# Kernel optimization log

Measured on AMD Instinct MI355X. Metric: run time of the kernel, lower is better.

The kernel has to match this reference:

```python
import jax, jax.numpy as jnp
import numpy as np

DIM = 1024
HEADS = 8
DIM_HEAD = 128
SCALE = DIM_HEAD ** -0.5
EPS = 1e-10
ROPE_THETA = 10000.0


def _rope_cos_sin(n, d, dtype):
    # lucidrains rotary-embedding-torch: interleaved freqs, repeated pairwise
    inv_freq = 1.0 / (ROPE_THETA ** (jnp.arange(0, d, 2, dtype=jnp.float32) / d))
    freqs = jnp.arange(n, dtype=jnp.float32)[:, None] * inv_freq[None, :]  # [n, d/2]
    freqs = jnp.repeat(freqs, 2, axis=-1)  # [n, d] interleaved (f0,f0,f1,f1,...)
    return jnp.cos(freqs).astype(dtype), jnp.sin(freqs).astype(dtype)


def _rotate_half(x):
    x = x.reshape(*x.shape[:-1], -1, 2)
    x1, x2 = x[..., 0], x[..., 1]
    return jnp.stack((-x2, x1), axis=-1).reshape(*x.shape[:-2], -1)


def _apply_rope(t, cos, sin):
    return t * cos + _rotate_half(t) * sin


def setup_inputs() -> dict:
    key = jax.random.key(0)
    k1, k2, k3, k4, k5 = jax.random.split(key, 5)
    b, n = 2, 2048
    return {
        "x": jax.random.normal(k1, (b, n, DIM), dtype=jnp.float32),
        "gamma": jnp.ones((DIM,), dtype=jnp.float32),
        "w_qkv": jax.random.normal(k2, (3 * HEADS * DIM_HEAD, DIM), dtype=jnp.float32) * 0.02,
        "w_out": jax.random.normal(k3, (DIM, HEADS * DIM_HEAD), dtype=jnp.float32) * 0.02,
        "head_gates": jnp.ones((HEADS,), dtype=jnp.float32) * 10.0,
        "mem_kv": jax.random.normal(k4, (b, HEADS, DIM_HEAD, DIM_HEAD), dtype=jnp.float32),
        "mem_norm": jax.random.uniform(k5, (b, HEADS, DIM_HEAD), dtype=jnp.float32) + 0.5,
    }


def _retrieve(t, mem_kv, mem_norm):
    # t: [b,h,n,dk] -> [b,h,n,dv]
    numer = jnp.einsum('bhnk,bhkv->bhnv', t, mem_kv)
    denom = jnp.einsum('bhnk,bhk->bhn', t, mem_norm)
    return numer / jnp.clip(denom, EPS, None)[..., None]


def reference(x, gamma, w_qkv, w_out, head_gates, mem_kv, mem_norm):
    b, n, _ = x.shape
    # RMSNorm (F.normalize * sqrt(dim) * gamma)
    xn = x / jnp.clip(jnp.linalg.norm(x, axis=-1, keepdims=True), 1e-12, None)
    xn = xn * (DIM ** 0.5) * gamma
    # qkv projection, split heads: 'b n (qkv h d) -> qkv b h n d'
    qkv = xn @ w_qkv.T  # [b,n,3*h*d]
    qkv = qkv.reshape(b, n, 3, HEADS, DIM_HEAD).transpose(2, 0, 3, 1, 4)
    q, k, v = qkv[0], qkv[1], qkv[2]

    cos, sin = _rope_cos_sin(n, DIM_HEAD, x.dtype)
    q_rot = _apply_rope(q * SCALE, cos, sin)
    k_rot = _apply_rope(k, cos, sin)

    sim = jnp.einsum('bhid,bhjd->bhij', q_rot, k_rot)
    causal = jnp.triu(jnp.ones((n, n), dtype=bool), 1)
    sim = jnp.where(causal, jnp.finfo(sim.dtype).min, sim)
    attn = jax.nn.softmax(sim, axis=-1)
    out = jnp.einsum('bhij,bhjd->bhid', attn, v)

    # linear-attention feature map on UNrotated, unscaled q/k
    qf = jax.nn.elu(q) + 1.0
    kf = jax.nn.elu(k) + 1.0

    # gated retrieval from past memories
    mem_out = _retrieve(qf, mem_kv, mem_norm)
    gates = jax.nn.sigmoid(head_gates)[None, :, None, None]
    out = out * gates + mem_out * (1.0 - gates)

    out = out.transpose(0, 2, 1, 3).reshape(b, n, HEADS * DIM_HEAD)
    out = out @ w_out.T

    # delta rule memory update
    delta_v = _retrieve(kf, mem_kv, mem_norm)
    v_new = v - delta_v
    new_kv = jnp.einsum('bhnk,bhnv->bhkv', kf, v_new) + mem_kv
    new_norm = kf.sum(axis=2) + mem_norm
    return out, new_kv, new_norm
```

## Files before the change

kernel.cpp:

```cpp
#include <hip/hip_runtime.h>
#include <hip/hip_bf16.h>

#define B_ 2
#define N_ 2048
#define H_ 8
#define DH_ 128
#define D_ 1024
#define NO_ 3072
#define SCALE_ 0.08838834764831845f

typedef __bf16 bf16;
typedef __bf16 bf16x4 __attribute__((ext_vector_type(4)));
typedef __bf16 bf16x8 __attribute__((ext_vector_type(8)));
typedef float f32x4 __attribute__((ext_vector_type(4)));

__device__ inline f32x4 mfma16(bf16x8 a, bf16x8 b, f32x4 c) {
  return __builtin_amdgcn_mfma_f32_16x16x32_bf16(a, b, c, 0, 0, 0);
}

__device__ inline float elu1(float x) { return x > 0.f ? x + 1.f : __expf(x); }

__device__ inline void gl_lds16(const bf16* g, bf16* l) {
  __builtin_amdgcn_global_load_lds(
      (const __attribute__((address_space(1))) unsigned int*)g,
      (__attribute__((address_space(3))) unsigned int*)l, 16, 0, 0);
}

__global__ __launch_bounds__(256) void k_rmsnorm(const float* __restrict__ x,
                                                 const float* __restrict__ gamma,
                                                 bf16* __restrict__ xn) {
  int row = blockIdx.x;
  int t = threadIdx.x;
  const float4* xr = (const float4*)(x + (size_t)row * D_);
  float4 xv = xr[t];
  float ss = xv.x*xv.x + xv.y*xv.y + xv.z*xv.z + xv.w*xv.w;
#pragma unroll
  for (int m = 1; m < 64; m <<= 1) ss += __shfl_xor(ss, m);
  __shared__ float sred[4];
  if ((t & 63) == 0) sred[t >> 6] = ss;
  __syncthreads();
  float tot = sred[0] + sred[1] + sred[2] + sred[3];
  float scale = 32.0f / fmaxf(sqrtf(tot), 1e-12f);
  float4 gv = ((const float4*)gamma)[t];
  bf16x4 ov;
  ov[0] = (bf16)(xv.x * scale * gv.x);
  ov[1] = (bf16)(xv.y * scale * gv.y);
  ov[2] = (bf16)(xv.z * scale * gv.z);
  ov[3] = (bf16)(xv.w * scale * gv.w);
  *(bf16x4*)(xn + (size_t)row * D_ + t * 4) = ov;
}

__global__ void k_cvt4(const float4* __restrict__ in, bf16x4* __restrict__ out, int n4) {
  int i = blockIdx.x * blockDim.x + threadIdx.x;
  if (i < n4) {
    float4 v = in[i];
    bf16x4 o;
    o[0] = (bf16)v.x; o[1] = (bf16)v.y; o[2] = (bf16)v.z; o[3] = (bf16)v.w;
    out[i] = o;
  }
}

__global__ __launch_bounds__(256) void k_mkvT(const float* __restrict__ mem_kv,
                                              bf16* __restrict__ mkvT) {
  int bh = blockIdx.x;
  int t = threadIdx.x;
  int v = t & 127, khalf = t >> 7;
  const float* src = mem_kv + (size_t)bh * DH_ * DH_;
  bf16* dst = mkvT + (size_t)bh * DH_ * DH_ + (size_t)v * DH_ + khalf * 64;
#pragma unroll
  for (int kk8 = 0; kk8 < 8; kk8++) {
    int k0 = khalf * 64 + kk8 * 8;
    bf16x8 o;
#pragma unroll
    for (int e = 0; e < 8; e++) o[e] = (bf16)src[(size_t)(k0 + e) * DH_ + v];
    *(bf16x8*)(dst + kk8 * 8) = o;
  }
}

template <typename OT>
__global__ __launch_bounds__(256) void k_gemm_lds(const bf16* __restrict__ A,
                                                  const bf16* __restrict__ B,
                                                  OT* __restrict__ C,
                                                  int M, int Nn, int K) {
  __shared__ __align__(16) bf16 sA[128 * 32];
  __shared__ __align__(16) bf16 sB[128 * 32];
  int t = threadIdx.x;
  int w = t >> 6, lane = t & 63, quad = lane >> 4, l16 = lane & 15;
  int m0 = blockIdx.y * 128, n0 = blockIdx.x * 128;
  int wr = (w & 1) * 64, wc = (w >> 1) * 64;
  f32x4 zf = {0.f, 0.f, 0.f, 0.f};
  f32x4 acc[4][4];
#pragma unroll
  for (int a = 0; a < 4; a++)
#pragma unroll
    for (int c = 0; c < 4; c++) acc[a][c] = zf;
  int srow = w * 16 + (lane >> 2);
  int scol = (lane & 3) * 8;
  const bf16* gA = A + (size_t)(m0 + srow) * K + scol;
  const bf16* gB = B + (size_t)(n0 + srow) * K + scol;
  bf16* lA0 = sA + (size_t)w * 16 * 32;
  bf16* lA1 = sA + (size_t)(64 + w * 16) * 32;
  bf16* lB0 = sB + (size_t)w * 16 * 32;
  bf16* lB1 = sB + (size_t)(64 + w * 16) * 32;
  for (int k0 = 0; k0 < K; k0 += 32) {
    __syncthreads();
    gl_lds16(gA + k0, lA0);
    gl_lds16(gA + (size_t)64 * K + k0, lA1);
    gl_lds16(gB + k0, lB0);
    gl_lds16(gB + (size_t)64 * K + k0, lB1);
    __syncthreads();
    bf16x8 af[4], bfr[4];
#pragma unroll
    for (int mt = 0; mt < 4; mt++)
      af[mt] = *(const bf16x8*)(sA + (wr + mt * 16 + l16) * 32 + quad * 8);
#pragma unroll
    for (int nt = 0; nt < 4; nt++)
      bfr[nt] = *(const bf16x8*)(sB + (wc + nt * 16 + l16) * 32 + quad * 8);
#pragma unroll
    for (int mt = 0; mt < 4; mt++)
#pragma unroll
      for (int nt = 0; nt < 4; nt++)
        acc[mt][nt] = mfma16(af[mt], bfr[nt], acc[mt][nt]);
  }
#pragma unroll
  for (int mt = 0; mt < 4; mt++)
#pragma unroll
    for (int nt = 0; nt < 4; nt++) {
      int row = m0 + wr + mt * 16 + quad * 4;
      int col = n0 + wc + nt * 16 + l16;
      OT* cp = C + (size_t)row * Nn + col;
#pragma unroll
      for (int r = 0; r < 4; r++) cp[(size_t)r * Nn] = (OT)acc[mt][nt][r];
    }
}

__global__ __launch_bounds__(256) void k_prep2(const bf16* __restrict__ qkv,
                                               const float* __restrict__ mem_norm,
                                               bf16* __restrict__ qr, bf16* __restrict__ kr,
                                               bf16* __restrict__ vT, bf16* __restrict__ kfT,
                                               float* __restrict__ qden, float* __restrict__ kden) {
  __shared__ __align__(16) bf16 sQ[64 * 136], sK[64 * 136], sV[64 * 136];
  __shared__ float smn[128];
  int n0 = blockIdx.x * 64, h = blockIdx.y, b = blockIdx.z;
  size_t bh = (size_t)b * H_ + h;
  int t = threadIdx.x;
#pragma unroll
  for (int p = 0; p < 4; p++) {
    int i = p * 256 + t;
    int row = i >> 4, c16 = i & 15;
    size_t base = ((size_t)b * N_ + n0 + row) * NO_ + (size_t)h * DH_;
    ((uint4*)sQ)[row * 17 + c16] = *((const uint4*)(qkv + base) + c16);
    ((uint4*)sK)[row * 17 + c16] = *((const uint4*)(qkv + base + D_) + c16);
    ((uint4*)sV)[row * 17 + c16] = *((const uint4*)(qkv + base + 2 * D_) + c16);
  }
  if (t < 128) smn[t] = mem_norm[bh * DH_ + t];
  __syncthreads();
  int row = t >> 1, h2 = t & 1, d0 = h2 * 64;
  int n = n0 + row;
  float sq = 0.f, sk = 0.f;
  const float cexp = 13.287712379549449f / 128.0f;
#pragma unroll 2
  for (int c = 0; c < 8; c++) {
    bf16x8 q8 = *(const bf16x8*)(sQ + row * 136 + d0 + c * 8);
    bf16x8 k8 = *(const bf16x8*)(sK + row * 136 + d0 + c * 8);
    bf16x8 qo, ko, kf8;
#pragma unroll
    for (int e = 0; e < 8; e += 2) {
      int d = d0 + c * 8 + e;
      float invf = exp2f(-(float)d * cexp);
      float ang = (float)n * invf;
      float sn, cs;
      __sincosf(ang, &sn, &cs);
      float qx = (float)q8[e] * SCALE_, qy = (float)q8[e + 1] * SCALE_;
      qo[e]     = (bf16)(qx * cs - qy * sn);
      qo[e + 1] = (bf16)(qy * cs + qx * sn);
      float kx = (float)k8[e], ky = (float)k8[e + 1];
      ko[e]     = (bf16)(kx * cs - ky * sn);
      ko[e + 1] = (bf16)(ky * cs + kx * sn);
      float f0 = elu1(kx), f1 = elu1(ky);
      kf8[e] = (bf16)f0; kf8[e + 1] = (bf16)f1;
      sk += f0 * smn[d] + f1 * smn[d + 1];
      sq += elu1((float)q8[e]) * smn[d] + elu1((float)q8[e + 1]) * smn[d + 1];
    }
    *(bf16x8*)(qr + (bh * N_ + n) * DH_ + d0 + c * 8) = qo;
    *(bf16x8*)(kr + (bh * N_ + n) * DH_ + d0 + c * 8) = ko;
    *(bf16x8*)(sK + row * 136 + d0 + c * 8) = kf8;
  }
  sq += __shfl_xor(sq, 1);
  sk += __shfl_xor(sk, 1);
  if (h2 == 0) { qden[bh * N_ + n] = sq; kden[bh * N_ + n] = sk; }
  __syncthreads();
  int d = t >> 1, part = t & 1;
#pragma unroll
  for (int v8 = 0; v8 < 4; v8++) {
    bf16x8 okf, ov;
#pragma unroll
    for (int e = 0; e < 8; e++) {
      int nn = part * 32 + v8 * 8 + e;
      okf[e] = sK[nn * 136 + d];
      ov[e]  = sV[nn * 136 + d];
    }
    size_t o = (bh * DH_ + d) * N_ + n0 + part * 32 + v8 * 8;
    *(bf16x8*)(kfT + o) = okf;
    *(bf16x8*)(vT + o)  = ov;
  }
}

__global__ __launch_bounds__(256) void k_attn2(const bf16* __restrict__ qr,
                                               const bf16* __restrict__ kr,
                                               const bf16* __restrict__ vT,
                                               bf16* __restrict__ attn_out,
                                               bf16* __restrict__ pO,
                                               float* __restrict__ pstat) {
  __shared__ __align__(16) bf16 sK[64 * 128];
  __shared__ __align__(16) bf16 sV[128 * 64];
  int L = blockIdx.x;
  int x = (L & 7) * 160 + (L >> 3);
  size_t bh = x / 80;
  int e = x % 80;
  int qt, c;
  if (e < 32)      { qt = 31 - (e >> 2); c = e & 3; }
  else if (e < 56) { int u = e - 32; qt = 23 - u / 3; c = u % 3; }
  else if (e < 72) { int u = e - 56; qt = 15 - (u >> 1); c = u & 1; }
  else             { qt = 7 - (e - 72); c = 0; }
  int jt0 = c * 8;
  int jt1 = min(jt0 + 8, qt + 1);

  int t = threadIdx.x;
  int w = t >> 6, lane = t & 63, quad = lane >> 4, l16 = lane & 15;
  int qlo = qt * 64 + w * 16;

  bf16x8 qfrag[4];
  const bf16* qrow = qr + (bh * N_ + qlo + l16) * DH_;
#pragma unroll
  for (int s = 0; s < 4; s++) qfrag[s] = *(const bf16x8*)(qrow + s * 32 + quad * 8);

  f32x4 zf = {0.f, 0.f, 0.f, 0.f};
  f32x4 o[8];
#pragma unroll
  for (int i = 0; i < 8; i++) o[i] = zf;
  float mrow = -1e30f, lrow = 0.f;

  int krow = lane >> 4, kc16 = lane & 15;
  int vrow = lane >> 3, vc8 = lane & 7;

  for (int jt = jt0; jt < jt1; jt++) {
    __syncthreads();
#pragma unroll
    for (int j = 0; j < 4; j++) {
      int prow = w * 16 + j * 4 + krow;
      int grow = (prow & 32) | ((prow & 12) << 1) | ((prow & 16) >> 2) | (prow & 3);
      const bf16* src = kr + (bh * N_ + (size_t)jt * 64 + grow) * DH_ + (kc16 ^ (prow & 7)) * 8;
      gl_lds16(src, sK + (w * 16 + j * 4) * 128);
    }
#pragma unroll
    for (int j = 0; j < 4; j++) {
      int row = w * 32 + j * 8 + vrow;
      const bf16* src = vT + (bh * DH_ + row) * N_ + (size_t)jt * 64 + (vc8 ^ (row & 7)) * 8;
      gl_lds16(src, sV + (w * 32 + j * 8) * 64);
    }
    __syncthreads();

    f32x4 sf[4];
#pragma unroll
    for (int nt = 0; nt < 4; nt++) sf[nt] = zf;
    __builtin_amdgcn_s_setprio(1);
#pragma unroll
    for (int s = 0; s < 4; s++) {
#pragma unroll
      for (int nt = 0; nt < 4; nt++) {
        int row = nt * 16 + l16;
        bf16x8 kf = *(const bf16x8*)(sK + row * 128 + ((s * 32 + quad * 8) ^ ((row & 7) << 3)));
        sf[nt] = mfma16(kf, qfrag[s], sf[nt]);
      }
    }
    __builtin_amdgcn_s_setprio(0);
    if (jt == qt) {
      int qg = qlo + l16;
#pragma unroll
      for (int nt = 0; nt < 4; nt++) {
        int kb = jt * 64 + ((nt >> 1) << 5) + (quad << 3) + ((nt & 1) << 2);
#pragma unroll
        for (int r = 0; r < 4; r++) {
          if (kb + r > qg) sf[nt][r] = -1e30f;
        }
      }
    }
    float tm = -1e30f;
#pragma unroll
    for (int nt = 0; nt < 4; nt++)
#pragma unroll
      for (int r = 0; r < 4; r++) tm = fmaxf(tm, sf[nt][r]);
    tm = fmaxf(tm, __shfl_xor(tm, 16));
    tm = fmaxf(tm, __shfl_xor(tm, 32));
    float mn = fmaxf(mrow, tm);
    float alpha = __expf(mrow - mn);
    float rs = 0.f;
#pragma unroll
    for (int nt = 0; nt < 4; nt++)
#pragma unroll
      for (int r = 0; r < 4; r++) {
        float p = __expf(sf[nt][r] - mn);
        sf[nt][r] = p;
        rs += p;
      }
    rs += __shfl_xor(rs, 16);
    rs += __shfl_xor(rs, 32);
    lrow = lrow * alpha + rs;
    mrow = mn;
#pragma unroll
    for (int i = 0; i < 8; i++) {
      o[i][0] *= alpha; o[i][1] *= alpha;
      o[i][2] *= alpha; o[i][3] *= alpha;
    }
    bf16x8 pa0, pa1;
#pragma unroll
    for (int r = 0; r < 4; r++) {
      pa0[r]     = (bf16)sf[0][r];
      pa0[4 + r] = (bf16)sf[1][r];
      pa1[r]     = (bf16)sf[2][r];
      pa1[4 + r] = (bf16)sf[3][r];
    }
    __builtin_amdgcn_s_setprio(1);
#pragma unroll
    for (int vt = 0; vt < 8; vt++) {
      int row0 = vt * 16 + l16;
      bf16x8 b0 = *(const bf16x8*)(sV + row0 * 64 + ((quad * 8) ^ ((row0 & 7) << 3)));
      bf16x8 b1 = *(const bf16x8*)(sV + row0 * 64 + ((32 + quad * 8) ^ ((row0 & 7) << 3)));
      o[vt] = mfma16(b0, pa0, o[vt]);
      o[vt] = mfma16(b1, pa1, o[vt]);
    }
    __builtin_amdgcn_s_setprio(0);
  }

  if (qt < 8) {
    float inv = 1.f / lrow;
    int qg = qlo + l16;
#pragma unroll
    for (int vt = 0; vt < 8; vt++) {
      bf16x4 ov;
#pragma unroll
      for (int r = 0; r < 4; r++) ov[r] = (bf16)(o[vt][r] * inv);
      *(bf16x4*)(attn_out + (bh * N_ + qg) * DH_ + vt * 16 + quad * 4) = ov;
    }
  } else {
    int cid = ((int)bh * 24 + qt - 8) * 4 + c;
    int lr = w * 16 + l16;
    if (quad == 0) {
      float2 st = {mrow, lrow};
      *(float2*)(pstat + ((size_t)cid * 64 + lr) * 2) = st;
    }
#pragma unroll
    for (int vt = 0; vt < 8; vt++) {
      bf16x4 ov;
#pragma unroll
      for (int r = 0; r < 4; r++) ov[r] = (bf16)o[vt][r];
      *(bf16x4*)(pO + ((size_t)cid * 64 + lr) * DH_ + vt * 16 + quad * 4) = ov;
    }
  }
}

__global__ __launch_bounds__(256) void k_combine(const bf16* __restrict__ pO,
                                                 const float* __restrict__ pstat,
                                                 bf16* __restrict__ attn_out) {
  int x = blockIdx.x;
  int bh = x / 24, qi = x % 24;
  int qt = 8 + qi;
  int nch = (qt + 8) / 8;
  int t = threadIdx.x;
  int row = t >> 2, dseg = (t & 3) * 32;
  int cidb = (bh * 24 + qi) * 4;
  float ms[4], ls[4];
  float mg = -1e30f;
#pragma unroll 4
  for (int c = 0; c < nch; c++) {
    float2 st = *(const float2*)(pstat + ((size_t)(cidb + c) * 64 + row) * 2);
    ms[c] = st.x; ls[c] = st.y;
    mg = fmaxf(mg, st.x);
  }
  float L = 0.f, wc[4];
#pragma unroll 4
  for (int c = 0; c < nch; c++) { wc[c] = __expf(ms[c] - mg); L += ls[c] * wc[c]; }
  float inv = 1.f / L;
  float acc[32];
#pragma unroll
  for (int i = 0; i < 32; i++) acc[i] = 0.f;
#pragma unroll 4
  for (int c = 0; c < nch; c++) {
    const bf16x8* p = (const bf16x8*)(pO + ((size_t)(cidb + c) * 64 + row) * DH_ + dseg);
#pragma unroll
    for (int j = 0; j < 4; j++) {
      bf16x8 v = p[j];
#pragma unroll
      for (int e2 = 0; e2 < 8; e2++) acc[j * 8 + e2] += wc[c] * (float)v[e2];
    }
  }
  bf16* dst = attn_out + ((size_t)bh * N_ + qt * 64 + row) * DH_ + dseg;
#pragma unroll
  for (int j = 0; j < 4; j++) {
    bf16x8 ov;
#pragma unroll
    for (int e2 = 0; e2 < 8; e2++) ov[e2] = (bf16)(acc[j * 8 + e2] * inv);
    *(bf16x8*)(dst + j * 8) = ov;
  }
}

#define SMT_STRIDE 136
#define VNSTR 138
__global__ __launch_bounds__(256) void k_retrieve2(const bf16* __restrict__ qkv,
                                                   const bf16* __restrict__ mkvT,
                                                   const float* __restrict__ qden,
                                                   const float* __restrict__ kden,
                                                   const bf16* __restrict__ attn,
                                                   const float* __restrict__ hg,
                                                   bf16* __restrict__ comb,
                                                   bf16* __restrict__ vnT) {
  __shared__ __align__(16) bf16 smT[DH_ * SMT_STRIDE];
  __shared__ bf16 sVn[64 * VNSTR];
  int h = blockIdx.y, b = blockIdx.z;
  size_t bh = (size_t)b * H_ + h;
  int t = threadIdx.x;
  int w = t >> 6, lane = t & 63, quad = lane >> 4, l16 = lane & 15;
  int n0 = blockIdx.x * 64;

  {
    const uint4* src = (const uint4*)(mkvT + bh * DH_ * DH_);
    uint4* dst = (uint4*)smT;
#pragma unroll
    for (int it = 0; it < 8; it++) {
      int i = t + it * 256;
      int row = i >> 4, col = i & 15;
      dst[row * 17 + col] = src[i];
    }
  }

  int nrow = n0 + w * 16 + l16;
  const bf16* base = qkv + ((size_t)b * N_ + nrow) * NO_ + h * DH_;
  bf16x8 qa[4], ka[4];
#pragma unroll
  for (int s = 0; s < 4; s++) {
    int k0 = s * 32 + quad * 8;
    bf16x8 q8 = *(const bf16x8*)(base + k0);
    bf16x8 k8 = *(const bf16x8*)(base + D_ + k0);
    bf16x8 qo, ko;
#pragma unroll
    for (int e2 = 0; e2 < 8; e2++) {
      qo[e2] = (bf16)elu1((float)q8[e2]);
      ko[e2] = (bf16)elu1((float)k8[e2]);
    }
    qa[s] = qo; ka[s] = ko;
  }

  __syncthreads();
  f32x4 zf = {0.f, 0.f, 0.f, 0.f};
  f32x4 accq[8], acck[8];
#pragma unroll
  for (int vt = 0; vt < 8; vt++) { accq[vt] = zf; acck[vt] = zf; }
#pragma unroll
  for (int vt = 0; vt < 8; vt++) {
#pragma unroll
    for (int s = 0; s < 4; s++) {
      bf16x8 bfr = *(const bf16x8*)(smT + (vt * 16 + l16) * SMT_STRIDE + s * 32 + quad * 8);
      accq[vt] = mfma16(qa[s], bfr, accq[vt]);
      acck[vt] = mfma16(ka[s], bfr, acck[vt]);
    }
  }

  float g = 1.f / (1.f + __expf(-hg[h]));
#pragma unroll
  for (int r = 0; r < 4; r++) {
    int nl = w * 16 + quad * 4 + r;
    int n = n0 + nl;
    size_t m = (size_t)b * N_ + n;
    float qd = fmaxf(qden[bh * N_ + n], 1e-10f);
    float kd = fmaxf(kden[bh * N_ + n], 1e-10f);
#pragma unroll
    for (int vt = 0; vt < 8; vt++) {
      int v = vt * 16 + l16;
      float mo = accq[vt][r] / qd;
      float ov = (float)attn[(bh * N_ + n) * DH_ + v];
      comb[m * D_ + h * DH_ + v] = (bf16)(ov * g + mo * (1.f - g));
      float vv = (float)qkv[m * NO_ + 2 * D_ + h * DH_ + v];
      sVn[nl * VNSTR + v] = (bf16)(vv - acck[vt][r] / kd);
    }
  }
  __syncthreads();
  int d = t >> 1, part = t & 1;
#pragma unroll
  for (int v8 = 0; v8 < 4; v8++) {
    bf16x8 ov;
#pragma unroll
    for (int e2 = 0; e2 < 8; e2++) ov[e2] = sVn[(part * 32 + v8 * 8 + e2) * VNSTR + d];
    *(bf16x8*)(vnT + (bh * DH_ + d) * N_ + n0 + part * 32 + v8 * 8) = ov;
  }
}

__global__ void k_init_kv(const float* __restrict__ mem_kv, float* __restrict__ out_kv) {
  int i = blockIdx.x * 256 + threadIdx.x;
  if (i < B_ * H_ * DH_ * DH_) out_kv[i] = mem_kv[i];
}

#define GSTR 40
__global__ __launch_bounds__(256) void k_newkv2(const bf16* __restrict__ kfT,
                                                const bf16* __restrict__ vnT,
                                                float* __restrict__ out_kv) {
  __shared__ __align__(16) bf16 sA[128 * GSTR];
  __shared__ __align__(16) bf16 sB[128 * GSTR];
  int t = threadIdx.x;
  int w = t >> 6, lane = t & 63, quad = lane >> 4, l16 = lane & 15;
  size_t bh = (size_t)blockIdx.z * H_ + blockIdx.y;
  const bf16* A  = kfT + bh * DH_ * N_;
  const bf16* Bm = vnT + bh * DH_ * N_;
  int wr = (w & 1) * 64, wc = (w >> 1) * 64;
  f32x4 zf = {0.f, 0.f, 0.f, 0.f};
  f32x4 acc[4][4];
#pragma unroll
  for (int a = 0; a < 4; a++)
#pragma unroll
    for (int c = 0; c < 4; c++) acc[a][c] = zf;
  int trow = t >> 2, tc = t & 3;
  int kend = (blockIdx.x + 1) * 128;
  for (int k0 = blockIdx.x * 128; k0 < kend; k0 += 32) {
    __syncthreads();
    ((uint4*)sA)[trow * 5 + tc]        = *((const uint4*)(A + (size_t)trow * N_ + k0) + tc);
    ((uint4*)sA)[(trow + 64) * 5 + tc] = *((const uint4*)(A + (size_t)(trow + 64) * N_ + k0) + tc);
    ((uint4*)sB)[trow * 5 + tc]        = *((const uint4*)(Bm + (size_t)trow * N_ + k0) + tc);
    ((uint4*)sB)[(trow + 64) * 5 + tc] = *((const uint4*)(Bm + (size_t)(trow + 64) * N_ + k0) + tc);
    __syncthreads();
    bf16x8 af[4], bfr[4];
#pragma unroll
    for (int mt = 0; mt < 4; mt++)
      af[mt] = *(const bf16x8*)(sA + (wr + mt * 16 + l16) * GSTR + quad * 8);
#pragma unroll
    for (int nt = 0; nt < 4; nt++)
      bfr[nt] = *(const bf16x8*)(sB + (wc + nt * 16 + l16) * GSTR + quad * 8);
#pragma unroll
    for (int mt = 0; mt < 4; mt++)
#pragma unroll
      for (int nt = 0; nt < 4; nt++)
        acc[mt][nt] = mfma16(af[mt], bfr[nt], acc[mt][nt]);
  }
  float* obh = out_kv + bh * DH_ * DH_;
#pragma unroll
  for (int mt = 0; mt < 4; mt++)
#pragma unroll
    for (int nt = 0; nt < 4; nt++) {
      int row = wr + mt * 16 + quad * 4;
      int col = wc + nt * 16 + l16;
#pragma unroll
      for (int r = 0; r < 4; r++)
        atomicAdd(obh + (size_t)(row + r) * DH_ + col, acc[mt][nt][r]);
    }
}

__global__ __launch_bounds__(256) void k_newnorm2(const bf16* __restrict__ kfT,
                                                  const float* __restrict__ mem_norm,
                                                  float* __restrict__ out_norm) {
  int bh = blockIdx.x;
  int t = threadIdx.x;
  int k = t >> 1, half = t & 1;
  const bf16x8* row = (const bf16x8*)(kfT + ((size_t)bh * DH_ + k) * N_ + half * (N_ / 2));
  float s = 0.f;
#pragma unroll 4
  for (int i = 0; i < N_ / 16; i++) {
    bf16x8 v = row[i];
#pragma unroll
    for (int e = 0; e < 8; e++) s += (float)v[e];
  }
  s += __shfl_xor(s, 1);
  if (half == 0) out_norm[(size_t)bh * DH_ + k] = mem_norm[(size_t)bh * DH_ + k] + s;
}

extern "C" void kernel_launch(void* const* d_in, const int* in_sizes, int n_in,
                              void* d_out, int out_size, void* d_ws, size_t ws_size,
                              hipStream_t stream) {
  const float* x        = (const float*)d_in[0];
  const float* gamma    = (const float*)d_in[1];
  const float* w_qkv    = (const float*)d_in[2];
  const float* w_out    = (const float*)d_in[3];
  const float* hg       = (const float*)d_in[4];
  const float* mem_kv   = (const float*)d_in[5];
  const float* mem_norm = (const float*)d_in[6];
  float* out      = (float*)d_out;
  float* out_kv   = out + (size_t)B_ * N_ * D_;
  float* out_norm = out_kv + (size_t)B_ * H_ * DH_ * DH_;

  char* ws = (char*)d_ws;
  size_t off = 0;
  auto alloc = [&](size_t bytes) -> void* {
    void* p = ws + off;
    off += (bytes + 255) & ~(size_t)255;
    return p;
  };
  bf16*  xn   = (bf16*)alloc((size_t)B_ * N_ * D_ * 2);
  bf16*  wqb  = (bf16*)alloc((size_t)NO_ * D_ * 2);
  bf16*  wob  = (bf16*)alloc((size_t)D_ * D_ * 2);
  bf16*  qkvb = (bf16*)alloc((size_t)B_ * N_ * NO_ * 2);
  bf16*  qr   = (bf16*)alloc((size_t)B_ * H_ * N_ * DH_ * 2);
  bf16*  kr   = (bf16*)alloc((size_t)B_ * H_ * N_ * DH_ * 2);
  bf16*  vT   = (bf16*)alloc((size_t)B_ * H_ * DH_ * N_ * 2);
  bf16*  kfT  = (bf16*)alloc((size_t)B_ * H_ * DH_ * N_ * 2);
  float* qden = (float*)alloc((size_t)B_ * H_ * N_ * 4);
  float* kden = (float*)alloc((size_t)B_ * H_ * N_ * 4);
  bf16*  attnb= (bf16*)alloc((size_t)B_ * H_ * N_ * DH_ * 2);
  bf16*  mkvT = (bf16*)alloc((size_t)B_ * H_ * DH_ * DH_ * 2);
  size_t pO_bytes    = (size_t)1536 * 64 * DH_ * 2;
  size_t pstat_bytes = (size_t)1536 * 64 * 2 * 4;
  size_t comb_bytes  = (size_t)B_ * N_ * D_ * 2;
  size_t vnT_bytes   = (size_t)B_ * H_ * DH_ * N_ * 2;
  size_t union_bytes = pO_bytes + pstat_bytes;
  if (comb_bytes + vnT_bytes > union_bytes) union_bytes = comb_bytes + vnT_bytes;
  char* uni = (char*)alloc(union_bytes);
  bf16*  pO    = (bf16*)uni;
  float* pstat = (float*)(uni + pO_bytes);
  bf16*  comb  = (bf16*)uni;
  bf16*  vnT   = (bf16*)(uni + comb_bytes);
  (void)in_sizes; (void)n_in; (void)out_size; (void)ws_size;

  k_rmsnorm<<<dim3(B_ * N_), 256, 0, stream>>>(x, gamma, xn);
  k_cvt4<<<(NO_ * D_ / 4 + 255) / 256, 256, 0, stream>>>((const float4*)w_qkv, (bf16x4*)wqb, NO_ * D_ / 4);
  k_cvt4<<<(D_ * D_ / 4 + 255) / 256, 256, 0, stream>>>((const float4*)w_out, (bf16x4*)wob, D_ * D_ / 4);
  k_mkvT<<<dim3(B_ * H_), 256, 0, stream>>>(mem_kv, mkvT);
  k_gemm_lds<bf16><<<dim3(NO_ / 128, B_ * N_ / 128), 256, 0, stream>>>(xn, wqb, qkvb, B_ * N_, NO_, D_);
  k_prep2<<<dim3(N_ / 64, H_, B_), 256, 0, stream>>>(qkvb, mem_norm, qr, kr, vT, kfT, qden, kden);
  k_attn2<<<dim3(1280), 256, 0, stream>>>(qr, kr, vT, attnb, pO, pstat);
  k_combine<<<dim3(384), 256, 0, stream>>>(pO, pstat, attnb);
  k_retrieve2<<<dim3(N_ / 64, H_, B_), 256, 0, stream>>>(qkvb, mkvT, qden, kden, attnb, hg, comb, vnT);
  k_gemm_lds<float><<<dim3(D_ / 128, B_ * N_ / 128), 256, 0, stream>>>(comb, wob, out, B_ * N_, D_, D_);
  k_init_kv<<<(B_ * H_ * DH_ * DH_ + 255) / 256, 256, 0, stream>>>(mem_kv, out_kv);
  k_newkv2<<<dim3(16, H_, B_), 256, 0, stream>>>(kfT, vnT, out_kv);
  k_newnorm2<<<dim3(B_ * H_), 256, 0, stream>>>(kfT, mem_norm, out_norm);
}
```

Measured before the change: 285.9 us.

## Fuse small kernels and add lazy softmax rescale in attention

Merges the two weight-conversion launches into one kernel. It folds the out_kv/out_norm initialisation into the mem_kv transpose kernel and computes the norm sum inside the new-kv GEMM with atomics, which removes three launches. Separately, the attention inner loop now skips the running-max update and accumulator rescale unless the tile max exceeds the stored max by more than 8. That saves exps and multiplies but leaves unnormalised exponentials up to e^8 in bf16 P values. The norm atomics make that output's summation order nondeterministic.

New measurement: 279.9 us. 1.02x faster.

```diff
diff --git a/kernel.cpp b/kernel.cpp
--- a/kernel.cpp
+++ b/kernel.cpp
@@ -50,18 +50,30 @@
   *(bf16x4*)(xn + (size_t)row * D_ + t * 4) = ov;
 }
 
-__global__ void k_cvt4(const float4* __restrict__ in, bf16x4* __restrict__ out, int n4) {
+__global__ void k_cvtW(const float4* __restrict__ a, bf16x4* __restrict__ oa, int na4,
+                       const float4* __restrict__ b, bf16x4* __restrict__ ob, int nb4) {
   int i = blockIdx.x * blockDim.x + threadIdx.x;
-  if (i < n4) {
-    float4 v = in[i];
+  if (i < na4) {
+    float4 v = a[i];
     bf16x4 o;
     o[0] = (bf16)v.x; o[1] = (bf16)v.y; o[2] = (bf16)v.z; o[3] = (bf16)v.w;
-    out[i] = o;
+    oa[i] = o;
+  } else {
+    int j = i - na4;
+    if (j < nb4) {
+      float4 v = b[j];
+      bf16x4 o;
+      o[0] = (bf16)v.x; o[1] = (bf16)v.y; o[2] = (bf16)v.z; o[3] = (bf16)v.w;
+      ob[j] = o;
+    }
   }
 }
 
 __global__ __launch_bounds__(256) void k_mkvT(const float* __restrict__ mem_kv,
-                                              bf16* __restrict__ mkvT) {
+                                              const float* __restrict__ mem_norm,
+                                              bf16* __restrict__ mkvT,
+                                              float* __restrict__ out_kv,
+                                              float* __restrict__ out_norm) {
   int bh = blockIdx.x;
   int t = threadIdx.x;
   int v = t & 127, khalf = t >> 7;
@@ -75,6 +87,11 @@
     for (int e = 0; e < 8; e++) o[e] = (bf16)src[(size_t)(k0 + e) * DH_ + v];
     *(bf16x8*)(dst + kk8 * 8) = o;
   }
+  const float4* s4 = (const float4*)src;
+  float4* d4 = (float4*)(out_kv + (size_t)bh * DH_ * DH_);
+#pragma unroll
+  for (int i = 0; i < 16; i++) d4[t + i * 256] = s4[t + i * 256];
+  if (t < DH_) out_norm[(size_t)bh * DH_ + t] = mem_norm[(size_t)bh * DH_ + t];
 }
 
 template <typename OT>
@@ -293,25 +310,40 @@
       for (int r = 0; r < 4; r++) tm = fmaxf(tm, sf[nt][r]);
     tm = fmaxf(tm, __shfl_xor(tm, 16));
     tm = fmaxf(tm, __shfl_xor(tm, 32));
-    float mn = fmaxf(mrow, tm);
-    float alpha = __expf(mrow - mn);
-    float rs = 0.f;
-#pragma unroll
-    for (int nt = 0; nt < 4; nt++)
-#pragma unroll
-      for (int r = 0; r < 4; r++) {
-        float p = __expf(sf[nt][r] - mn);
-        sf[nt][r] = p;
-        rs += p;
+    if (__any(tm > mrow + 8.f)) {
+      float mn = fmaxf(mrow, tm);
+      float alpha = __expf(mrow - mn);
+      float rs = 0.f;
+#pragma unroll
+      for (int nt = 0; nt < 4; nt++)
+#pragma unroll
+        for (int r = 0; r < 4; r++) {
+          float p = __expf(sf[nt][r] - mn);
+          sf[nt][r] = p;
+          rs += p;
+        }
+      rs += __shfl_xor(rs, 16);
+      rs += __shfl_xor(rs, 32);
+      lrow = lrow * alpha + rs;
+      mrow = mn;
+#pragma unroll
+      for (int i = 0; i < 8; i++) {
+        o[i][0] *= alpha; o[i][1] *= alpha;
+        o[i][2] *= alpha; o[i][3] *= alpha;
       }
-    rs += __shfl_xor(rs, 16);
-    rs += __shfl_xor(rs, 32);
-    lrow = lrow * alpha + rs;
-    mrow = mn;
-#pragma unroll
-    for (int i = 0; i < 8; i++) {
-      o[i][0] *= alpha; o[i][1] *= alpha;
-      o[i][2] *= alpha; o[i][3] *= alpha;
+    } else {
+      float rs = 0.f;
+#pragma unroll
+      for (int nt = 0; nt < 4; nt++)
+#pragma unroll
+        for (int r = 0; r < 4; r++) {
+          float p = __expf(sf[nt][r] - mrow);
+          sf[nt][r] = p;
+          rs += p;
+        }
+      rs += __shfl_xor(rs, 16);
+      rs += __shfl_xor(rs, 32);
+      lrow += rs;
     }
     bf16x8 pa0, pa1;
 #pragma unroll
@@ -495,15 +527,11 @@
   }
 }
 
-__global__ void k_init_kv(const float* __restrict__ mem_kv, float* __restrict__ out_kv) {
-  int i = blockIdx.x * 256 + threadIdx.x;
-  if (i < B_ * H_ * DH_ * DH_) out_kv[i] = mem_kv[i];
-}
-
 #define GSTR 40
 __global__ __launch_bounds__(256) void k_newkv2(const bf16* __restrict__ kfT,
                                                 const bf16* __restrict__ vnT,
-                                                float* __restrict__ out_kv) {
+                                                float* __restrict__ out_kv,
+                                                float* __restrict__ out_norm) {
   __shared__ __align__(16) bf16 sA[128 * GSTR];
   __shared__ __align__(16) bf16 sB[128 * GSTR];
   int t = threadIdx.x;
@@ -519,13 +547,19 @@
 #pragma unroll
     for (int c = 0; c < 4; c++) acc[a][c] = zf;
   int trow = t >> 2, tc = t & 3;
+  float sn0 = 0.f, sn1 = 0.f;
   int kend = (blockIdx.x + 1) * 128;
   for (int k0 = blockIdx.x * 128; k0 < kend; k0 += 32) {
     __syncthreads();
-    ((uint4*)sA)[trow * 5 + tc]        = *((const uint4*)(A + (size_t)trow * N_ + k0) + tc);
-    ((uint4*)sA)[(trow + 64) * 5 + tc] = *((const uint4*)(A + (size_t)(trow + 64) * N_ + k0) + tc);
+    uint4 va0 = *((const uint4*)(A + (size_t)trow * N_ + k0) + tc);
+    uint4 va1 = *((const uint4*)(A + (size_t)(trow + 64) * N_ + k0) + tc);
+    ((uint4*)sA)[trow * 5 + tc]        = va0;
+    ((uint4*)sA)[(trow + 64) * 5 + tc] = va1;
     ((uint4*)sB)[trow * 5 + tc]        = *((const uint4*)(Bm + (size_t)trow * N_ + k0) + tc);
     ((uint4*)sB)[(trow + 64) * 5 + tc] = *((const uint4*)(Bm + (size_t)(trow + 64) * N_ + k0) + tc);
+    bf16x8 x0 = *(bf16x8*)&va0, x1 = *(bf16x8*)&va1;
+#pragma unroll
+    for (int e = 0; e < 8; e++) { sn0 += (float)x0[e]; sn1 += (float)x1[e]; }
     __syncthreads();
     bf16x8 af[4], bfr[4];
 #pragma unroll
@@ -539,6 +573,12 @@
 #pragma unroll
       for (int nt = 0; nt < 4; nt++)
         acc[mt][nt] = mfma16(af[mt], bfr[nt], acc[mt][nt]);
+  }
+  sn0 += __shfl_xor(sn0, 1); sn0 += __shfl_xor(sn0, 2);
+  sn1 += __shfl_xor(sn1, 1); sn1 += __shfl_xor(sn1, 2);
+  if (tc == 0) {
+    atomicAdd(out_norm + bh * DH_ + trow, sn0);
+    atomicAdd(out_norm + bh * DH_ + trow + 64, sn1);
   }
   float* obh = out_kv + bh * DH_ * DH_;
 #pragma unroll
@@ -551,24 +591,6 @@
       for (int r = 0; r < 4; r++)
         atomicAdd(obh + (size_t)(row + r) * DH_ + col, acc[mt][nt][r]);
     }
-}
-
-__global__ __launch_bounds__(256) void k_newnorm2(const bf16* __restrict__ kfT,
-                                                  const float* __restrict__ mem_norm,
-                                                  float* __restrict__ out_norm) {
-  int bh = blockIdx.x;
-  int t = threadIdx.x;
-  int k = t >> 1, half = t & 1;
-  const bf16x8* row = (const bf16x8*)(kfT + ((size_t)bh * DH_ + k) * N_ + half * (N_ / 2));
-  float s = 0.f;
-#pragma unroll 4
-  for (int i = 0; i < N_ / 16; i++) {
-    bf16x8 v = row[i];
-#pragma unroll
-    for (int e = 0; e < 8; e++) s += (float)v[e];
-  }
-  s += __shfl_xor(s, 1);
-  if (half == 0) out_norm[(size_t)bh * DH_ + k] = mem_norm[(size_t)bh * DH_ + k] + s;
 }
 
 extern "C" void kernel_launch(void* const* d_in, const int* in_sizes, int n_in,
@@ -618,16 +640,15 @@
   (void)in_sizes; (void)n_in; (void)out_size; (void)ws_size;
 
   k_rmsnorm<<<dim3(B_ * N_), 256, 0, stream>>>(x, gamma, xn);
-  k_cvt4<<<(NO_ * D_ / 4 + 255) / 256, 256, 0, stream>>>((const float4*)w_qkv, (bf16x4*)wqb, NO_ * D_ / 4);
-  k_cvt4<<<(D_ * D_ / 4 + 255) / 256, 256, 0, stream>>>((const float4*)w_out, (bf16x4*)wob, D_ * D_ / 4);
-  k_mkvT<<<dim3(B_ * H_), 256, 0, stream>>>(mem_kv, mkvT);
+  k_cvtW<<<(NO_ * D_ / 4 + D_ * D_ / 4 + 255) / 256, 256, 0, stream>>>(
+      (const float4*)w_qkv, (bf16x4*)wqb, NO_ * D_ / 4,
+      (const float4*)w_out, (bf16x4*)wob, D_ * D_ / 4);
+  k_mkvT<<<dim3(B_ * H_), 256, 0, stream>>>(mem_kv, mem_norm, mkvT, out_kv, out_norm);
   k_gemm_lds<bf16><<<dim3(NO_ / 128, B_ * N_ / 128), 256, 0, stream>>>(xn, wqb, qkvb, B_ * N_, NO_, D_);
   k_prep2<<<dim3(N_ / 64, H_, B_), 256, 0, stream>>>(qkvb, mem_norm, qr, kr, vT, kfT, qden, kden);
   k_attn2<<<dim3(1280), 256, 0, stream>>>(qr, kr, vT, attnb, pO, pstat);
   k_combine<<<dim3(384), 256, 0, stream>>>(pO, pstat, attnb);
   k_retrieve2<<<dim3(N_ / 64, H_, B_), 256, 0, stream>>>(qkvb, mkvT, qden, kden, attnb, hg, comb, vnT);
   k_gemm_lds<float><<<dim3(D_ / 128, B_ * N_ / 128), 256, 0, stream>>>(comb, wob, out, B_ * N_, D_, D_);
-  k_init_kv<<<(B_ * H_ * DH_ * DH_ + 255) / 256, 256, 0, stream>>>(mem_kv, out_kv);
-  k_newkv2<<<dim3(16, H_, B_), 256, 0, stream>>>(kfT, vnT, out_kv);
-  k_newnorm2<<<dim3(B_ * H_), 256, 0, stream>>>(kfT, mem_norm, out_norm);
-}
+  k_newkv2<<<dim3(16, H_, B_), 256, 0, stream>>>(kfT, vnT, out_kv, out_norm);
+}
```
